# Kernel optimization log

Measured on AMD Instinct MI355X. Metric: run time of the kernel, lower is better.

## Reference

```python
import jax, jax.numpy as jnp
import numpy as np

H = 4  # heads


def _tconv(x, src, dst, ea, Wq, bq, Wk, bk, Wv, bv, We, Ws, bs):
    # PyG TransformerConv, heads=4, concat=False, root_weight=True, beta=False
    N = x.shape[0]
    Dh = Wq.shape[1] // H  # per-head dim (= hidden_channels)
    q = (x @ Wq + bq).reshape(N, H, Dh)
    k = (x @ Wk + bk).reshape(N, H, Dh)
    v = (x @ Wv + bv).reshape(N, H, Dh)
    e = (ea @ We).reshape(-1, H, Dh)      # lin_edge has no bias in PyG
    kj = k[src] + e                        # [E, H, Dh]
    vj = v[src] + e                        # [E, H, Dh]
    alpha = (q[dst] * kj).sum(-1) / jnp.sqrt(jnp.asarray(Dh, x.dtype))  # [E, H]
    # segment softmax over incoming edges of each dst node
    m = jax.ops.segment_max(alpha, dst, num_segments=N)
    a = jnp.exp(alpha - m[dst])
    s = jax.ops.segment_sum(a, dst, num_segments=N)
    a = a / (s[dst] + 1e-16)
    out = jax.ops.segment_sum(a[:, :, None] * vj, dst, num_segments=N)  # [N, H, Dh]
    out = out.mean(axis=1)                 # concat=False -> mean over heads
    return out + x @ Ws + bs               # root/skip connection


def setup_inputs() -> dict:
    key = jax.random.key(0)
    ks = jax.random.split(key, 32)
    N, E, C_in, C_e, Ch = 50000, 800000, 32, 16, 32
    d = {}
    d['x'] = jax.random.normal(ks[0], (N, C_in), dtype=jnp.float32)
    d['edge_attr'] = jax.random.normal(ks[1], (E, C_e), dtype=jnp.float32)
    d['edge_index'] = jax.random.randint(ks[2], (2, E), 0, N, dtype=jnp.int32)
    s = 0.05
    i = 3
    for L, cin in ((1, C_in), (2, Ch)):
        d[f'Wq{L}'] = jax.random.normal(ks[i], (cin, H * Ch)) * s; i += 1
        d[f'bq{L}'] = jnp.zeros((H * Ch,), jnp.float32)
        d[f'Wk{L}'] = jax.random.normal(ks[i], (cin, H * Ch)) * s; i += 1
        d[f'bk{L}'] = jnp.zeros((H * Ch,), jnp.float32)
        d[f'Wv{L}'] = jax.random.normal(ks[i], (cin, H * Ch)) * s; i += 1
        d[f'bv{L}'] = jnp.zeros((H * Ch,), jnp.float32)
        d[f'We{L}'] = jax.random.normal(ks[i], (C_e, H * Ch)) * s; i += 1
        d[f'Ws{L}'] = jax.random.normal(ks[i], (cin, Ch)) * s; i += 1
        d[f'bs{L}'] = jnp.zeros((Ch,), jnp.float32)
    d['Wm1'] = jax.random.normal(ks[i], (2 * Ch + C_e, Ch)) * s; i += 1
    d['bm1'] = jnp.zeros((Ch,), jnp.float32)
    d['Wm2'] = jax.random.normal(ks[i], (Ch, 1)) * s; i += 1
    d['bm2'] = jnp.zeros((1,), jnp.float32)
    return d


def reference(x, edge_attr, edge_index,
              Wq1, bq1, Wk1, bk1, Wv1, bv1, We1, Ws1, bs1,
              Wq2, bq2, Wk2, bk2, Wv2, bv2, We2, Ws2, bs2,
              Wm1, bm1, Wm2, bm2):
    src, dst = edge_index[0], edge_index[1]
    h = jax.nn.relu(_tconv(x, src, dst, edge_attr, Wq1, bq1, Wk1, bk1, Wv1, bv1, We1, Ws1, bs1))
    h = jax.nn.relu(_tconv(h, src, dst, edge_attr, Wq2, bq2, Wk2, bk2, Wv2, bv2, We2, Ws2, bs2))
    ef = jnp.concatenate([h[src], edge_attr, h[dst]], axis=-1)  # [E, 2*Ch + C_e]
    out = jax.nn.relu(ef @ Wm1 + bm1) @ Wm2 + bm2
    return out.reshape(-1)
```

## Files before the change

### kernel.cpp

```cpp
#include <hip/hip_runtime.h>
#include <math.h>

#define D128 128
#define CH32 32
#define CE16 16

static __device__ __forceinline__ float red32(float t) {
    t += __shfl_xor(t, 1);
    t += __shfl_xor(t, 2);
    t += __shfl_xor(t, 4);
    t += __shfl_xor(t, 8);
    t += __shfl_xor(t, 16);
    return t;
}

__global__ void k_hist(const int* __restrict__ dst, int* __restrict__ deg, int E) {
    int e = blockIdx.x * blockDim.x + threadIdx.x;
    if (e < E) atomicAdd(&deg[dst[e]], 1);
}

__global__ void k_scan1(const int* __restrict__ deg, int* __restrict__ offs,
                        int* __restrict__ bsum, int N) {
    __shared__ int buf[256];
    int t = threadIdx.x;
    int i = blockIdx.x * 256 + t;
    int v = (i < N) ? deg[i] : 0;
    buf[t] = v;
    __syncthreads();
    #pragma unroll
    for (int off = 1; off < 256; off <<= 1) {
        int val = (t >= off) ? buf[t - off] : 0;
        __syncthreads();
        buf[t] += val;
        __syncthreads();
    }
    if (i < N) offs[i] = buf[t] - v;
    if (t == 255) bsum[blockIdx.x] = buf[255];
}

__global__ void k_scan2(const int* __restrict__ bsum, int* __restrict__ boff, int nb) {
    __shared__ int buf[256];
    int t = threadIdx.x;
    int v = (t < nb) ? bsum[t] : 0;
    buf[t] = v;
    __syncthreads();
    #pragma unroll
    for (int off = 1; off < 256; off <<= 1) {
        int val = (t >= off) ? buf[t - off] : 0;
        __syncthreads();
        buf[t] += val;
        __syncthreads();
    }
    if (t < nb) boff[t] = buf[t] - v;
}

__global__ void k_scan3(const int* __restrict__ boff, int* __restrict__ offs,
                        int* __restrict__ cur, int N, int E) {
    int i = blockIdx.x * blockDim.x + threadIdx.x;
    if (i < N) {
        int o = offs[i] + boff[i >> 8];
        offs[i] = o;
        cur[i] = o;
    }
    if (i == 0) offs[N] = E;
}

__global__ void k_scatter(const int* __restrict__ src, const int* __restrict__ dst,
                          int* __restrict__ cur, int* __restrict__ csr_srcb,
                          float4* __restrict__ ea_csr4, const float4* __restrict__ ea4,
                          int E) {
    int e = blockIdx.x * blockDim.x + threadIdx.x;
    if (e < E) {
        int d = dst[e];
        int p = atomicAdd(&cur[d], 1);
        csr_srcb[p] = src[e] << 10;
        float4 a0 = ea4[e * 4 + 0];
        float4 a1 = ea4[e * 4 + 1];
        float4 a2 = ea4[e * 4 + 2];
        float4 a3 = ea4[e * 4 + 3];
        ea_csr4[p * 4 + 0] = a0;
        ea_csr4[p * 4 + 1] = a1;
        ea_csr4[p * 4 + 2] = a2;
        ea_csr4[p * 4 + 3] = a3;
    }
}

__global__ __launch_bounds__(128) void k_nodeproj(
    const float* __restrict__ xin,
    const float* __restrict__ Wq, const float* __restrict__ bq,
    const float* __restrict__ Wk, const float* __restrict__ bk,
    const float* __restrict__ Wv, const float* __restrict__ bv,
    const float* __restrict__ Ws, const float* __restrict__ bs,
    float* __restrict__ q, float* __restrict__ kv,
    float* __restrict__ skip, int N)
{
    int tid = threadIdx.x;
    int c   = tid & 31;
    float wq[32], wk[32], wv[32], ws[32];
    #pragma unroll
    for (int j = 0; j < 32; j++) {
        wq[j] = Wq[j * D128 + tid];
        wk[j] = Wk[j * D128 + tid];
        wv[j] = Wv[j * D128 + tid];
        ws[j] = Ws[j * CH32 + c];
    }
    float bqc = bq[tid], bkc = bk[tid], bvc = bv[tid], bsc = bs[c];
    __shared__ float xs[4][32];
    int nchunk = (N + 3) / 4;
    for (int chk = blockIdx.x; chk < nchunk; chk += gridDim.x) {
        int base = chk * 4;
        {
            int r = tid >> 5;
            int n = base + r;
            xs[r][c] = (n < N) ? xin[n * 32 + c] : 0.f;
        }
        __syncthreads();
        #pragma unroll
        for (int r = 0; r < 4; r++) {
            int n = base + r;
            if (n < N) {
                float aq = bqc, ak = bkc, av = bvc;
                #pragma unroll
                for (int j = 0; j < 32; j++) {
                    float xj = xs[r][j];
                    aq = fmaf(xj, wq[j], aq);
                    ak = fmaf(xj, wk[j], ak);
                    av = fmaf(xj, wv[j], av);
                }
                q[n * D128 + tid] = aq;
                kv[(size_t)n * 256 + tid]       = ak;
                kv[(size_t)n * 256 + 128 + tid] = av;
            }
        }
        {
            int r = tid >> 5;
            int n = base + r;
            if (n < N) {
                float as = bsc;
                #pragma unroll
                for (int j = 0; j < 32; j++) as = fmaf(xs[r][j], ws[j], as);
                skip[n * 32 + c] = as;
            }
        }
        __syncthreads();
    }
}

__global__ __launch_bounds__(128) void k_edgeattn(
    const float* __restrict__ q, const float* __restrict__ kv,
    const float* __restrict__ skip,
    const float* __restrict__ ea_csr, const float* __restrict__ We,
    const int* __restrict__ offs, const int* __restrict__ csr_srcb,
    float* __restrict__ hout)
{
    int node = blockIdx.x;
    int tid = threadIdx.x;
    __shared__ float red[128];

    float we[16];
    #pragma unroll
    for (int j = 0; j < 16; j++) we[j] = We[j * D128 + tid];

    float qv = q[(size_t)node * D128 + tid] * 0.17677669529663687f;
    int s0 = offs[node], s1 = offs[node + 1];

    float l = 0.f, acc = 0.f;
    const char* kvb = (const char*)kv;
    int toff = tid * 4;

    int i = s0;
    if ((s1 - s0) & 1) {
        int sa = csr_srcb[i];
        const char* pa = kvb + (size_t)(unsigned)sa + toff;
        float ka = *(const float*)(pa);
        float va = *(const float*)(pa + 512);
        const float4* ea4 = (const float4*)&ea_csr[(size_t)i * 16];
        float4 a0 = ea4[0], a1 = ea4[1], a2 = ea4[2], a3 = ea4[3];
        float eca;
        eca = a0.x * we[0];
        eca = fmaf(a0.y, we[1],  eca);
        eca = fmaf(a0.z, we[2],  eca);
        eca = fmaf(a0.w, we[3],  eca);
        eca = fmaf(a1.x, we[4],  eca);
        eca = fmaf(a1.y, we[5],  eca);
        eca = fmaf(a1.z, we[6],  eca);
        eca = fmaf(a1.w, we[7],  eca);
        eca = fmaf(a2.x, we[8],  eca);
        eca = fmaf(a2.y, we[9],  eca);
        eca = fmaf(a2.z, we[10], eca);
        eca = fmaf(a2.w, we[11], eca);
        eca = fmaf(a3.x, we[12], eca);
        eca = fmaf(a3.y, we[13], eca);
        eca = fmaf(a3.z, we[14], eca);
        eca = fmaf(a3.w, we[15], eca);
        float alpha = red32(qv * (ka + eca));
        float p = __expf(alpha);
        l += p;
        acc = fmaf(p, va + eca, acc);
        i++;
    }

    for (; i < s1; i += 2) {
        int sa = csr_srcb[i];
        int sb = csr_srcb[i + 1];
        const char* pa = kvb + (size_t)(unsigned)sa + toff;
        const char* pb = kvb + (size_t)(unsigned)sb + toff;
        float ka = *(const float*)(pa);
        float va = *(const float*)(pa + 512);
        float kb = *(const float*)(pb);
        float vb = *(const float*)(pb + 512);
        const float4* ea4 = (const float4*)&ea_csr[(size_t)i * 16];
        float4 a0 = ea4[0], a1 = ea4[1], a2 = ea4[2], a3 = ea4[3];
        float4 b0 = ea4[4], b1 = ea4[5], b2 = ea4[6], b3 = ea4[7];

        float eca, ecb;
        eca = a0.x * we[0];                 ecb = b0.x * we[0];
        eca = fmaf(a0.y, we[1],  eca);      ecb = fmaf(b0.y, we[1],  ecb);
        eca = fmaf(a0.z, we[2],  eca);      ecb = fmaf(b0.z, we[2],  ecb);
        eca = fmaf(a0.w, we[3],  eca);      ecb = fmaf(b0.w, we[3],  ecb);
        eca = fmaf(a1.x, we[4],  eca);      ecb = fmaf(b1.x, we[4],  ecb);
        eca = fmaf(a1.y, we[5],  eca);      ecb = fmaf(b1.y, we[5],  ecb);
        eca = fmaf(a1.z, we[6],  eca);      ecb = fmaf(b1.z, we[6],  ecb);
        eca = fmaf(a1.w, we[7],  eca);      ecb = fmaf(b1.w, we[7],  ecb);
        eca = fmaf(a2.x, we[8],  eca);      ecb = fmaf(b2.x, we[8],  ecb);
        eca = fmaf(a2.y, we[9],  eca);      ecb = fmaf(b2.y, we[9],  ecb);
        eca = fmaf(a2.z, we[10], eca);      ecb = fmaf(b2.z, we[10], ecb);
        eca = fmaf(a2.w, we[11], eca);      ecb = fmaf(b2.w, we[11], ecb);
        eca = fmaf(a3.x, we[12], eca);      ecb = fmaf(b3.x, we[12], ecb);
        eca = fmaf(a3.y, we[13], eca);      ecb = fmaf(b3.y, we[13], ecb);
        eca = fmaf(a3.z, we[14], eca);      ecb = fmaf(b3.z, we[14], ecb);
        eca = fmaf(a3.w, we[15], eca);      ecb = fmaf(b3.w, we[15], ecb);

        float kja = ka + eca, vja = va + eca;
        float kjb = kb + ecb, vjb = vb + ecb;

        float alpha0 = red32(qv * kja);
        float alpha1 = red32(qv * kjb);

        float p0 = __expf(alpha0);
        float p1 = __expf(alpha1);
        l += p0 + p1;
        acc = fmaf(p0, vja, acc);
        acc = fmaf(p1, vjb, acc);
    }

    red[tid] = acc / (l + 1e-16f);
    __syncthreads();
    if (tid < 32) {
        float o = 0.25f * (red[tid] + red[tid + 32] + red[tid + 64] + red[tid + 96])
                + skip[(size_t)node * 32 + tid];
        hout[(size_t)node * 32 + tid] = fmaxf(o, 0.f);
    }
}

__global__ __launch_bounds__(256) void k_mlp(
    const float* __restrict__ h, const float* __restrict__ ea,
    const int* __restrict__ src, const int* __restrict__ dst,
    const float* __restrict__ Wm1, const float* __restrict__ bm1,
    const float* __restrict__ Wm2, const float* __restrict__ bm2,
    float* __restrict__ out, int E)
{
    __shared__ float4 W4[80 * 8];
    __shared__ float bm1L[32];
    __shared__ float wm2L[32];
    int tid = threadIdx.x;
    const float4* Wm1_4 = (const float4*)Wm1;
    for (int i = tid; i < 640; i += 256) W4[i] = Wm1_4[i];
    if (tid < 32) { bm1L[tid] = bm1[tid]; wm2L[tid] = Wm2[tid]; }
    __syncthreads();

    int e = blockIdx.x * 256 + tid;
    if (e >= E) return;
    float b2 = bm2[0];
    int s = src[e], d = dst[e];

    float4 acc[8];
    #pragma unroll
    for (int i = 0; i < 8; i++) acc[i] = make_float4(0.f, 0.f, 0.f, 0.f);

    auto dorow = [&](int j, float xj) {
        #pragma unroll
        for (int c4 = 0; c4 < 8; c4++) {
            float4 w = W4[j * 8 + c4];
            acc[c4].x = fmaf(xj, w.x, acc[c4].x);
            acc[c4].y = fmaf(xj, w.y, acc[c4].y);
            acc[c4].z = fmaf(xj, w.z, acc[c4].z);
            acc[c4].w = fmaf(xj, w.w, acc[c4].w);
        }
    };

    const float4* hs  = (const float4*)(h + (size_t)s * 32);
    const float4* hd  = (const float4*)(h + (size_t)d * 32);
    const float4* eav = (const float4*)(ea + (size_t)e * 16);
    #pragma unroll
    for (int qd = 0; qd < 8; qd++) {
        float4 xv = hs[qd];
        dorow(qd * 4 + 0, xv.x); dorow(qd * 4 + 1, xv.y);
        dorow(qd * 4 + 2, xv.z); dorow(qd * 4 + 3, xv.w);
    }
    #pragma unroll
    for (int qd = 0; qd < 4; qd++) {
        float4 xv = eav[qd];
        dorow(32 + qd * 4 + 0, xv.x); dorow(32 + qd * 4 + 1, xv.y);
        dorow(32 + qd * 4 + 2, xv.z); dorow(32 + qd * 4 + 3, xv.w);
    }
    #pragma unroll
    for (int qd = 0; qd < 8; qd++) {
        float4 xv = hd[qd];
        dorow(48 + qd * 4 + 0, xv.x); dorow(48 + qd * 4 + 1, xv.y);
        dorow(48 + qd * 4 + 2, xv.z); dorow(48 + qd * 4 + 3, xv.w);
    }

    float y = b2;
    #pragma unroll
    for (int c4 = 0; c4 < 8; c4++) {
        y += fmaxf(acc[c4].x + bm1L[c4 * 4 + 0], 0.f) * wm2L[c4 * 4 + 0];
        y += fmaxf(acc[c4].y + bm1L[c4 * 4 + 1], 0.f) * wm2L[c4 * 4 + 1];
        y += fmaxf(acc[c4].z + bm1L[c4 * 4 + 2], 0.f) * wm2L[c4 * 4 + 2];
        y += fmaxf(acc[c4].w + bm1L[c4 * 4 + 3], 0.f) * wm2L[c4 * 4 + 3];
    }
    out[e] = y;
}

extern "C" void kernel_launch(void* const* d_in, const int* in_sizes, int n_in,
                              void* d_out, int out_size, void* d_ws, size_t ws_size,
                              hipStream_t stream)
{
    const float* x  = (const float*)d_in[0];
    const float* ea = (const float*)d_in[1];
    const int*   ei = (const int*)d_in[2];
    const int N = in_sizes[0] / 32;
    const int E = in_sizes[1] / 16;
    const int* src = ei;
    const int* dst = ei + E;

    const float *Wq1 = (const float*)d_in[3],  *bq1 = (const float*)d_in[4];
    const float *Wk1 = (const float*)d_in[5],  *bk1 = (const float*)d_in[6];
    const float *Wv1 = (const float*)d_in[7],  *bv1 = (const float*)d_in[8];
    const float *We1 = (const float*)d_in[9],  *Ws1 = (const float*)d_in[10];
    const float *bs1 = (const float*)d_in[11];
    const float *Wq2 = (const float*)d_in[12], *bq2 = (const float*)d_in[13];
    const float *Wk2 = (const float*)d_in[14], *bk2 = (const float*)d_in[15];
    const float *Wv2 = (const float*)d_in[16], *bv2 = (const float*)d_in[17];
    const float *We2 = (const float*)d_in[18], *Ws2 = (const float*)d_in[19];
    const float *bs2 = (const float*)d_in[20];
    const float *Wm1 = (const float*)d_in[21], *bm1 = (const float*)d_in[22];
    const float *Wm2 = (const float*)d_in[23], *bm2 = (const float*)d_in[24];

    char* w = (char*)d_ws;
    auto alloc = [&](size_t bytes) -> void* {
        void* p = (void*)w;
        w += (bytes + 255) & ~(size_t)255;
        return p;
    };
    int* deg      = (int*)alloc((size_t)N * 4);
    int* offs     = (int*)alloc(((size_t)N + 1) * 4);
    int* cur      = (int*)alloc((size_t)N * 4);
    int* bsum     = (int*)alloc(256 * 4);
    int* boff     = (int*)alloc(256 * 4);
    int* csr_srcb = (int*)alloc((size_t)E * 4);
    float* ea_csr = (float*)alloc((size_t)E * 16 * 4);
    float* qb     = (float*)alloc((size_t)N * 128 * 4);
    float* kvb    = (float*)alloc((size_t)N * 256 * 4);
    float* skipb  = (float*)alloc((size_t)N * 32 * 4);
    float* h1     = (float*)alloc((size_t)N * 32 * 4);
    float* h2     = (float*)alloc((size_t)N * 32 * 4);

    hipMemsetAsync(deg, 0, (size_t)N * 4, stream);

    int ebl = (E + 255) / 256;
    int nb  = (N + 255) / 256;
    k_hist<<<ebl, 256, 0, stream>>>(dst, deg, E);
    k_scan1<<<nb, 256, 0, stream>>>(deg, offs, bsum, N);
    k_scan2<<<1, 256, 0, stream>>>(bsum, boff, nb);
    k_scan3<<<nb, 256, 0, stream>>>(boff, offs, cur, N, E);
    k_scatter<<<ebl, 256, 0, stream>>>(src, dst, cur, csr_srcb,
                                       (float4*)ea_csr, (const float4*)ea, E);

    k_nodeproj<<<1024, 128, 0, stream>>>(x, Wq1, bq1, Wk1, bk1, Wv1, bv1, Ws1, bs1,
                                         qb, kvb, skipb, N);
    k_edgeattn<<<N, 128, 0, stream>>>(qb, kvb, skipb, ea_csr, We1,
                                      offs, csr_srcb, h1);
    k_nodeproj<<<1024, 128, 0, stream>>>(h1, Wq2, bq2, Wk2, bk2, Wv2, bv2, Ws2, bs2,
                                         qb, kvb, skipb, N);
    k_edgeattn<<<N, 128, 0, stream>>>(qb, kvb, skipb, ea_csr, We2,
                                      offs, csr_srcb, h2);
    k_mlp<<<ebl, 256, 0, stream>>>(h2, ea, src, dst, Wm1, bm1, Wm2, bm2,
                                   (float*)d_out, E);
}
```

Measured before the change: 609.1 us.

## Use one 64-lane wavefront per node with two channels per lane in edge attention

```diff
diff --git a/kernel.cpp b/kernel.cpp
--- a/kernel.cpp
+++ b/kernel.cpp
@@ -4,15 +4,6 @@
 #define D128 128
 #define CH32 32
 #define CE16 16
-
-static __device__ __forceinline__ float red32(float t) {
-    t += __shfl_xor(t, 1);
-    t += __shfl_xor(t, 2);
-    t += __shfl_xor(t, 4);
-    t += __shfl_xor(t, 8);
-    t += __shfl_xor(t, 16);
-    return t;
-}
 
 __global__ void k_hist(const int* __restrict__ dst, int* __restrict__ deg, int E) {
     int e = blockIdx.x * blockDim.x + threadIdx.x;
@@ -146,7 +137,7 @@
     }
 }
 
-__global__ __launch_bounds__(128) void k_edgeattn(
+__global__ __launch_bounds__(64) void k_edgeattn(
     const float* __restrict__ q, const float* __restrict__ kv,
     const float* __restrict__ skip,
     const float* __restrict__ ea_csr, const float* __restrict__ We,
@@ -154,49 +145,64 @@
     float* __restrict__ hout)
 {
     int node = blockIdx.x;
-    int tid = threadIdx.x;
-    __shared__ float red[128];
-
-    float we[16];
-    #pragma unroll
-    for (int j = 0; j < 16; j++) we[j] = We[j * D128 + tid];
-
-    float qv = q[(size_t)node * D128 + tid] * 0.17677669529663687f;
+    int lane = threadIdx.x;
+    int col2 = lane << 1;
+
+    float2 we[16];
+    #pragma unroll
+    for (int j = 0; j < 16; j++)
+        we[j] = *(const float2*)&We[j * D128 + col2];
+
+    const float QS = 0.17677669529663687f * 1.4426950408889634f;
+    float2 qv = *(const float2*)&q[(size_t)node * D128 + col2];
+    qv.x *= QS; qv.y *= QS;
+
     int s0 = offs[node], s1 = offs[node + 1];
 
-    float l = 0.f, acc = 0.f;
+    float l = 0.f;
+    float ac0 = 0.f, ac1 = 0.f;
     const char* kvb = (const char*)kv;
-    int toff = tid * 4;
+    int toff = lane * 8;
 
     int i = s0;
     if ((s1 - s0) & 1) {
         int sa = csr_srcb[i];
         const char* pa = kvb + (size_t)(unsigned)sa + toff;
-        float ka = *(const float*)(pa);
-        float va = *(const float*)(pa + 512);
+        float2 ka = *(const float2*)(pa);
+        float2 va = *(const float2*)(pa + 512);
         const float4* ea4 = (const float4*)&ea_csr[(size_t)i * 16];
         float4 a0 = ea4[0], a1 = ea4[1], a2 = ea4[2], a3 = ea4[3];
-        float eca;
-        eca = a0.x * we[0];
-        eca = fmaf(a0.y, we[1],  eca);
-        eca = fmaf(a0.z, we[2],  eca);
-        eca = fmaf(a0.w, we[3],  eca);
-        eca = fmaf(a1.x, we[4],  eca);
-        eca = fmaf(a1.y, we[5],  eca);
-        eca = fmaf(a1.z, we[6],  eca);
-        eca = fmaf(a1.w, we[7],  eca);
-        eca = fmaf(a2.x, we[8],  eca);
-        eca = fmaf(a2.y, we[9],  eca);
-        eca = fmaf(a2.z, we[10], eca);
-        eca = fmaf(a2.w, we[11], eca);
-        eca = fmaf(a3.x, we[12], eca);
-        eca = fmaf(a3.y, we[13], eca);
-        eca = fmaf(a3.z, we[14], eca);
-        eca = fmaf(a3.w, we[15], eca);
-        float alpha = red32(qv * (ka + eca));
-        float p = __expf(alpha);
+
+        float e0 = 0.f, e1 = 0.f;
+        e0 = fmaf(a0.x, we[0].x,  e0);  e1 = fmaf(a0.x, we[0].y,  e1);
+        e0 = fmaf(a0.y, we[1].x,  e0);  e1 = fmaf(a0.y, we[1].y,  e1);
+        e0 = fmaf(a0.z, we[2].x,  e0);  e1 = fmaf(a0.z, we[2].y,  e1);
+        e0 = fmaf(a0.w, we[3].x,  e0);  e1 = fmaf(a0.w, we[3].y,  e1);
+        e0 = fmaf(a1.x, we[4].x,  e0);  e1 = fmaf(a1.x, we[4].y,  e1);
+        e0 = fmaf(a1.y, we[5].x,  e0);  e1 = fmaf(a1.y, we[5].y,  e1);
+        e0 = fmaf(a1.z, we[6].x,  e0);  e1 = fmaf(a1.z, we[6].y,  e1);
+        e0 = fmaf(a1.w, we[7].x,  e0);  e1 = fmaf(a1.w, we[7].y,  e1);
+        e0 = fmaf(a2.x, we[8].x,  e0);  e1 = fmaf(a2.x, we[8].y,  e1);
+        e0 = fmaf(a2.y, we[9].x,  e0);  e1 = fmaf(a2.y, we[9].y,  e1);
+        e0 = fmaf(a2.z, we[10].x, e0);  e1 = fmaf(a2.z, we[10].y, e1);
+        e0 = fmaf(a2.w, we[11].x, e0);  e1 = fmaf(a2.w, we[11].y, e1);
+        e0 = fmaf(a3.x, we[12].x, e0);  e1 = fmaf(a3.x, we[12].y, e1);
+        e0 = fmaf(a3.y, we[13].x, e0);  e1 = fmaf(a3.y, we[13].y, e1);
+        e0 = fmaf(a3.z, we[14].x, e0);  e1 = fmaf(a3.z, we[14].y, e1);
+        e0 = fmaf(a3.w, we[15].x, e0);  e1 = fmaf(a3.w, we[15].y, e1);
+
+        float kj0 = ka.x + e0, kj1 = ka.y + e1;
+        float vj0 = va.x + e0, vj1 = va.y + e1;
+        float t = qv.x * kj0;
+        t = fmaf(qv.y, kj1, t);
+        t += __shfl_xor(t, 1);
+        t += __shfl_xor(t, 2);
+        t += __shfl_xor(t, 4);
+        t += __shfl_xor(t, 8);
+        float p = __builtin_amdgcn_exp2f(t);
         l += p;
-        acc = fmaf(p, va + eca, acc);
+        ac0 = fmaf(p, vj0, ac0);
+        ac1 = fmaf(p, vj1, ac1);
         i++;
     }
 
@@ -205,51 +211,82 @@
         int sb = csr_srcb[i + 1];
         const char* pa = kvb + (size_t)(unsigned)sa + toff;
         const char* pb = kvb + (size_t)(unsigned)sb + toff;
-        float ka = *(const float*)(pa);
-        float va = *(const float*)(pa + 512);
-        float kb = *(const float*)(pb);
-        float vb = *(const float*)(pb + 512);
+        float2 ka = *(const float2*)(pa);
+        float2 va = *(const float2*)(pa + 512);
+        float2 kb = *(const float2*)(pb);
+        float2 vb = *(const float2*)(pb + 512);
         const float4* ea4 = (const float4*)&ea_csr[(size_t)i * 16];
         float4 a0 = ea4[0], a1 = ea4[1], a2 = ea4[2], a3 = ea4[3];
         float4 b0 = ea4[4], b1 = ea4[5], b2 = ea4[6], b3 = ea4[7];
 
-        float eca, ecb;
-        eca = a0.x * we[0];                 ecb = b0.x * we[0];
-        eca = fmaf(a0.y, we[1],  eca);      ecb = fmaf(b0.y, we[1],  ecb);
-        eca = fmaf(a0.z, we[2],  eca);      ecb = fmaf(b0.z, we[2],  ecb);
-        eca = fmaf(a0.w, we[3],  eca);      ecb = fmaf(b0.w, we[3],  ecb);
-        eca = fmaf(a1.x, we[4],  eca);      ecb = fmaf(b1.x, we[4],  ecb);
-        eca = fmaf(a1.y, we[5],  eca);      ecb = fmaf(b1.y, we[5],  ecb);
-        eca = fmaf(a1.z, we[6],  eca);      ecb = fmaf(b1.z, we[6],  ecb);
-        eca = fmaf(a1.w, we[7],  eca);      ecb = fmaf(b1.w, we[7],  ecb);
-        eca = fmaf(a2.x, we[8],  eca);      ecb = fmaf(b2.x, we[8],  ecb);
-        eca = fmaf(a2.y, we[9],  eca);      ecb = fmaf(b2.y, we[9],  ecb);
-        eca = fmaf(a2.z, we[10], eca);      ecb = fmaf(b2.z, we[10], ecb);
-        eca = fmaf(a2.w, we[11], eca);      ecb = fmaf(b2.w, we[11], ecb);
-        eca = fmaf(a3.x, we[12], eca);      ecb = fmaf(b3.x, we[12], ecb);
-        eca = fmaf(a3.y, we[13], eca);      ecb = fmaf(b3.y, we[13], ecb);
-        eca = fmaf(a3.z, we[14], eca);      ecb = fmaf(b3.z, we[14], ecb);
-        eca = fmaf(a3.w, we[15], eca);      ecb = fmaf(b3.w, we[15], ecb);
-
-        float kja = ka + eca, vja = va + eca;
-        float kjb = kb + ecb, vjb = vb + ecb;
-
-        float alpha0 = red32(qv * kja);
-        float alpha1 = red32(qv * kjb);
-
-        float p0 = __expf(alpha0);
-        float p1 = __expf(alpha1);
+        float ea0 = 0.f, ea1 = 0.f, eb0 = 0.f, eb1 = 0.f;
+        ea0 = fmaf(a0.x, we[0].x,  ea0);  ea1 = fmaf(a0.x, we[0].y,  ea1);
+        eb0 = fmaf(b0.x, we[0].x,  eb0);  eb1 = fmaf(b0.x, we[0].y,  eb1);
+        ea0 = fmaf(a0.y, we[1].x,  ea0);  ea1 = fmaf(a0.y, we[1].y,  ea1);
+        eb0 = fmaf(b0.y, we[1].x,  eb0);  eb1 = fmaf(b0.y, we[1].y,  eb1);
+        ea0 = fmaf(a0.z, we[2].x,  ea0);  ea1 = fmaf(a0.z, we[2].y,  ea1);
+        eb0 = fmaf(b0.z, we[2].x,  eb0);  eb1 = fmaf(b0.z, we[2].y,  eb1);
+        ea0 = fmaf(a0.w, we[3].x,  ea0);  ea1 = fmaf(a0.w, we[3].y,  ea1);
+        eb0 = fmaf(b0.w, we[3].x,  eb0);  eb1 = fmaf(b0.w, we[3].y,  eb1);
+        ea0 = fmaf(a1.x, we[4].x,  ea0);  ea1 = fmaf(a1.x, we[4].y,  ea1);
+        eb0 = fmaf(b1.x, we[4].x,  eb0);  eb1 = fmaf(b1.x, we[4].y,  eb1);
+        ea0 = fmaf(a1.y, we[5].x,  ea0);  ea1 = fmaf(a1.y, we[5].y,  ea1);
+        eb0 = fmaf(b1.y, we[5].x,  eb0);  eb1 = fmaf(b1.y, we[5].y,  eb1);
+        ea0 = fmaf(a1.z, we[6].x,  ea0);  ea1 = fmaf(a1.z, we[6].y,  ea1);
+        eb0 = fmaf(b1.z, we[6].x,  eb0);  eb1 = fmaf(b1.z, we[6].y,  eb1);
+        ea0 = fmaf(a1.w, we[7].x,  ea0);  ea1 = fmaf(a1.w, we[7].y,  ea1);
+        eb0 = fmaf(b1.w, we[7].x,  eb0);  eb1 = fmaf(b1.w, we[7].y,  eb1);
+        ea0 = fmaf(a2.x, we[8].x,  ea0);  ea1 = fmaf(a2.x, we[8].y,  ea1);
+        eb0 = fmaf(b2.x, we[8].x,  eb0);  eb1 = fmaf(b2.x, we[8].y,  eb1);
+        ea0 = fmaf(a2.y, we[9].x,  ea0);  ea1 = fmaf(a2.y, we[9].y,  ea1);
+        eb0 = fmaf(b2.y, we[9].x,  eb0);  eb1 = fmaf(b2.y, we[9].y,  eb1);
+        ea0 = fmaf(a2.z, we[10].x, ea0);  ea1 = fmaf(a2.z, we[10].y, ea1);
+        eb0 = fmaf(b2.z, we[10].x, eb0);  eb1 = fmaf(b2.z, we[10].y, eb1);
+        ea0 = fmaf(a2.w, we[11].x, ea0);  ea1 = fmaf(a2.w, we[11].y, ea1);
+        eb0 = fmaf(b2.w, we[11].x, eb0);  eb1 = fmaf(b2.w, we[11].y, eb1);
+        ea0 = fmaf(a3.x, we[12].x, ea0);  ea1 = fmaf(a3.x, we[12].y, ea1);
+        eb0 = fmaf(b3.x, we[12].x, eb0);  eb1 = fmaf(b3.x, we[12].y, eb1);
+        ea0 = fmaf(a3.y, we[13].x, ea0);  ea1 = fmaf(a3.y, we[13].y, ea1);
+        eb0 = fmaf(b3.y, we[13].x, eb0);  eb1 = fmaf(b3.y, we[13].y, eb1);
+        ea0 = fmaf(a3.z, we[14].x, ea0);  ea1 = fmaf(a3.z, we[14].y, ea1);
+        eb0 = fmaf(b3.z, we[14].x, eb0);  eb1 = fmaf(b3.z, we[14].y, eb1);
+        ea0 = fmaf(a3.w, we[15].x, ea0);  ea1 = fmaf(a3.w, we[15].y, ea1);
+        eb0 = fmaf(b3.w, we[15].x, eb0);  eb1 = fmaf(b3.w, we[15].y, eb1);
+
+        float kja0 = ka.x + ea0, kja1 = ka.y + ea1;
+        float vja0 = va.x + ea0, vja1 = va.y + ea1;
+        float kjb0 = kb.x + eb0, kjb1 = kb.y + eb1;
+        float vjb0 = vb.x + eb0, vjb1 = vb.y + eb1;
+
+        float ta = qv.x * kja0;
+        float tb = qv.x * kjb0;
+        ta = fmaf(qv.y, kja1, ta);
+        tb = fmaf(qv.y, kjb1, tb);
+
+        ta += __shfl_xor(ta, 1);   tb += __shfl_xor(tb, 1);
+        ta += __shfl_xor(ta, 2);   tb += __shfl_xor(tb, 2);
+        ta += __shfl_xor(ta, 4);   tb += __shfl_xor(tb, 4);
+        ta += __shfl_xor(ta, 8);   tb += __shfl_xor(tb, 8);
+
+        float p0 = __builtin_amdgcn_exp2f(ta);
+        float p1 = __builtin_amdgcn_exp2f(tb);
         l += p0 + p1;
-        acc = fmaf(p0, vja, acc);
-        acc = fmaf(p1, vjb, acc);
-    }
-
-    red[tid] = acc / (l + 1e-16f);
-    __syncthreads();
-    if (tid < 32) {
-        float o = 0.25f * (red[tid] + red[tid + 32] + red[tid + 64] + red[tid + 96])
-                + skip[(size_t)node * 32 + tid];
-        hout[(size_t)node * 32 + tid] = fmaxf(o, 0.f);
+        ac0 = fmaf(p0, vja0, ac0);
+        ac1 = fmaf(p0, vja1, ac1);
+        ac0 = fmaf(p1, vjb0, ac0);
+        ac1 = fmaf(p1, vjb1, ac1);
+    }
+
+    float inv = 1.0f / (l + 1e-16f);
+    float r0 = ac0 * inv;
+    float r1 = ac1 * inv;
+    r0 += __shfl_xor(r0, 16);   r1 += __shfl_xor(r1, 16);
+    r0 += __shfl_xor(r0, 32);   r1 += __shfl_xor(r1, 32);
+    if (lane < 16) {
+        const float2 sk = *(const float2*)&skip[(size_t)node * 32 + col2];
+        float o0 = fmaxf(fmaf(0.25f, r0, sk.x), 0.f);
+        float o1 = fmaxf(fmaf(0.25f, r1, sk.y), 0.f);
+        *(float2*)&hout[(size_t)node * 32 + col2] = make_float2(o0, o1);
     }
 }
 
@@ -379,12 +416,12 @@
 
     k_nodeproj<<<1024, 128, 0, stream>>>(x, Wq1, bq1, Wk1, bk1, Wv1, bv1, Ws1, bs1,
                                          qb, kvb, skipb, N);
-    k_edgeattn<<<N, 128, 0, stream>>>(qb, kvb, skipb, ea_csr, We1,
-                                      offs, csr_srcb, h1);
+    k_edgeattn<<<N, 64, 0, stream>>>(qb, kvb, skipb, ea_csr, We1,
+                                     offs, csr_srcb, h1);
     k_nodeproj<<<1024, 128, 0, stream>>>(h1, Wq2, bq2, Wk2, bk2, Wv2, bv2, Ws2, bs2,
                                          qb, kvb, skipb, N);
-    k_edgeattn<<<N, 128, 0, stream>>>(qb, kvb, skipb, ea_csr, We2,
-                                      offs, csr_srcb, h2);
+    k_edgeattn<<<N, 64, 0, stream>>>(qb, kvb, skipb, ea_csr, We2,
+                                     offs, csr_srcb, h2);
     k_mlp<<<ebl, 256, 0, stream>>>(h2, ea, src, dst, Wm1, bm1, Wm2, bm2,
                                    (float*)d_out, E);
 }
```

After: 607.4 us. Within noise of the previous version (-0.3%).
